# Kernel optimization log

Hardware: AMD Instinct MI355X
Metric: run time of the kernel (lower is better)

The kernel has to match this reference:

```python
import jax, jax.numpy as jnp
import numpy as np


def setup_inputs() -> dict:
    key = jax.random.key(0)
    k1, k2, k3, k4, k5 = jax.random.split(key, 5)
    B, S, H, L = 32, 4096, 512, 2
    scale = 1.0 / np.sqrt(H)
    return {
        "out": jax.random.normal(k1, (B, S, H), dtype=jnp.float32),
        "hidden": jax.random.normal(k2, (L, B, H), dtype=jnp.float32),
        "W": jax.random.normal(k3, (H, H), dtype=jnp.float32) * scale,
        "b": jax.random.normal(k4, (H,), dtype=jnp.float32) * scale,
        "v": jax.random.normal(k5, (H,), dtype=jnp.float32) * scale,
    }


def reference(out, hidden, W, b, v):
    # hidden_last: (B, 1, H) from last layer
    h_last = hidden[-1][:, None, :]
    # energy = tanh(out @ W^T + b + h_last)  -> (B, S, H)
    energy = jnp.tanh(jnp.einsum("bsh,oh->bso", out, W) + b + h_last)
    # scores = energy @ v  -> (B, S)
    scores = jnp.einsum("bsh,h->bs", energy, v)
    attn = jax.nn.softmax(scores, axis=-1)
    # context = sum_s attn[b,s] * out[b,s,:]  -> (B, H)
    context = jnp.einsum("bs,bsh->bh", attn, out)
    return (context, attn)
```

## Files before the change

### kernel.cpp

```cpp
#include <hip/hip_runtime.h>
#include <hip/hip_bf16.h>

#define B_ 32
#define S_ 4096
#define H_ 512
#define M_ (B_ * S_)
#define L_ 2

typedef __bf16 bf16;
typedef bf16 bf16x8 __attribute__((ext_vector_type(8)));
typedef float floatx4 __attribute__((ext_vector_type(4)));
typedef float floatx16 __attribute__((ext_vector_type(16)));

__device__ inline bf16 f2b(float f) { return (bf16)f; }

__device__ inline float fast_tanh(float x) {
    float xc = fminf(15.0f, fmaxf(-15.0f, x));
    float e = __expf(2.0f * xc);
    return (e - 1.0f) * __builtin_amdgcn_rcpf(e + 1.0f);
}

__global__ __launch_bounds__(256) void convert_Wfrag(const float* __restrict__ W,
                                                     bf16* __restrict__ Wf) {
    int gid  = blockIdx.x * 256 + threadIdx.x;
    int lane = gid & 63;
    int ks   = (gid >> 6) & 31;
    int nt   = gid >> 11;
    int row  = nt * 32 + (lane & 31);
    int col  = ks * 16 + (lane >> 5) * 8;
    const float* src = W + (size_t)row * H_ + col;
    floatx4 f0 = *(const floatx4*)src;
    floatx4 f1 = *(const floatx4*)(src + 4);
    bf16x8 p = { f2b(f0[0]), f2b(f0[1]), f2b(f0[2]), f2b(f0[3]),
                 f2b(f1[0]), f2b(f1[1]), f2b(f1[2]), f2b(f1[3]) };
    *(bf16x8*)(Wf + (size_t)gid * 8) = p;
}

#define MT 64

__global__ __launch_bounds__(256, 2) void scores_kernel(
    const float* __restrict__ outT,
    const bf16*  __restrict__ Wf,
    const float* __restrict__ bias,
    const float* __restrict__ hidden,
    const float* __restrict__ v,
    float* __restrict__ scores)
{
    __shared__ bf16 Alds[MT * 512];

    const int tid  = threadIdx.x;
    const int wave = tid >> 6;
    const int lane = tid & 63;
    const int l31  = lane & 31;
    const int half = lane >> 5;

    const int m0    = blockIdx.x * MT;
    const int batch = m0 >> 12;

    {
        const floatx4* src = (const floatx4*)(outT + (size_t)m0 * H_);
        #pragma unroll 4
        for (int it = 0; it < 16; ++it) {
            int idx = it * 256 + tid;
            int r   = idx >> 6;
            int j   = idx & 63;
            floatx4 f0 = __builtin_nontemporal_load(src + idx * 2);
            floatx4 f1 = __builtin_nontemporal_load(src + idx * 2 + 1);
            bf16x8 p = { f2b(f0[0]), f2b(f0[1]), f2b(f0[2]), f2b(f0[3]),
                         f2b(f1[0]), f2b(f1[1]), f2b(f1[2]), f2b(f1[3]) };
            int frag = (r >> 5) * 32 + (j >> 1);
            int slot = (j & 1) * 32 + ((r + (j >> 1)) & 31);
            *(bf16x8*)&Alds[frag * 512 + slot * 8] = p;
        }
    }
    __syncthreads();

    const bf16* wf = Wf + (size_t)(wave * 4) * 32 * 512 + lane * 8;

    floatx16 acc[2][4];
    #pragma unroll
    for (int mt = 0; mt < 2; ++mt)
        #pragma unroll
        for (int nt = 0; nt < 4; ++nt)
            acc[mt][nt] = (floatx16)(0.0f);

    bf16x8 bb[4][4];
    bf16x8 aa[2][2];
    #pragma unroll
    for (int p = 0; p < 4; ++p)
        #pragma unroll
        for (int nt = 0; nt < 4; ++nt)
            bb[p][nt] = *(const bf16x8*)(wf + nt * 16384 + p * 512);
    #pragma unroll
    for (int mt = 0; mt < 2; ++mt)
        aa[0][mt] = *(const bf16x8*)
            &Alds[(mt * 32 + 0) * 512 + (half * 32 + (l31 & 31)) * 8];

    #pragma unroll
    for (int ks = 0; ks < 32; ++ks) {
        const int cur = ks & 3;
        const int ap  = ks & 1;
        if (ks < 31) {
            const int rot = (l31 + ks + 1) & 31;
            #pragma unroll
            for (int mt = 0; mt < 2; ++mt)
                aa[ap ^ 1][mt] = *(const bf16x8*)
                    &Alds[(mt * 32 + ks + 1) * 512 + (half * 32 + rot) * 8];
        }
        #pragma unroll
        for (int mt = 0; mt < 2; ++mt)
            #pragma unroll
            for (int nt = 0; nt < 4; ++nt)
                acc[mt][nt] = __builtin_amdgcn_mfma_f32_32x32x16_bf16(
                    aa[ap][mt], bb[cur][nt], acc[mt][nt], 0, 0, 0);
        if (ks < 28) {
            #pragma unroll
            for (int nt = 0; nt < 4; ++nt)
                bb[cur][nt] = *(const bf16x8*)(wf + nt * 16384 + (ks + 4) * 512);
        }
    }

    const float* hlast = hidden + (size_t)((L_ - 1) * B_ + batch) * H_;
    float part[2][16];
    #pragma unroll
    for (int mt = 0; mt < 2; ++mt)
        #pragma unroll
        for (int rg = 0; rg < 16; ++rg) part[mt][rg] = 0.0f;

    #pragma unroll
    for (int nt = 0; nt < 4; ++nt) {
        int n = wave * 128 + nt * 32 + l31;
        float bn = bias[n] + hlast[n];
        float vn = v[n];
        #pragma unroll
        for (int mt = 0; mt < 2; ++mt)
            #pragma unroll
            for (int rg = 0; rg < 16; ++rg)
                part[mt][rg] += fast_tanh(acc[mt][nt][rg] + bn) * vn;
    }

    __syncthreads();
    float* sred = (float*)Alds;
    #pragma unroll
    for (int mt = 0; mt < 2; ++mt)
        #pragma unroll
        for (int rg = 0; rg < 16; ++rg) {
            float s = part[mt][rg];
            s += __shfl_xor(s, 1);
            s += __shfl_xor(s, 2);
            s += __shfl_xor(s, 4);
            s += __shfl_xor(s, 8);
            s += __shfl_xor(s, 16);
            if (l31 == 0) {
                int row = (rg & 3) + 8 * (rg >> 2) + 4 * half;
                sred[wave * 64 + mt * 32 + row] = s;
            }
        }
    __syncthreads();
    if (tid < 64)
        scores[m0 + tid] = (sred[tid] + sred[64 + tid]) + (sred[128 + tid] + sred[192 + tid]);
}

__global__ __launch_bounds__(256) void softmax_kernel(const float* __restrict__ scores,
                                                      float* __restrict__ attn) {
    __shared__ float red[4];
    int b = blockIdx.x, tid = threadIdx.x;
    const float* row = scores + (size_t)b * S_;
    float vals[16];
    float mx = -3.4e38f;
    #pragma unroll
    for (int i = 0; i < 16; ++i) { vals[i] = row[i * 256 + tid]; mx = fmaxf(mx, vals[i]); }
    #pragma unroll
    for (int off = 32; off >= 1; off >>= 1) mx = fmaxf(mx, __shfl_xor(mx, off));
    if ((tid & 63) == 0) red[tid >> 6] = mx;
    __syncthreads();
    mx = fmaxf(fmaxf(red[0], red[1]), fmaxf(red[2], red[3]));
    __syncthreads();
    float sum = 0.f;
    #pragma unroll
    for (int i = 0; i < 16; ++i) { vals[i] = __expf(vals[i] - mx); sum += vals[i]; }
    #pragma unroll
    for (int off = 32; off >= 1; off >>= 1) sum += __shfl_xor(sum, off);
    if ((tid & 63) == 0) red[tid >> 6] = sum;
    __syncthreads();
    float inv = 1.0f / (red[0] + red[1] + red[2] + red[3]);
    #pragma unroll
    for (int i = 0; i < 16; ++i) attn[(size_t)b * S_ + i * 256 + tid] = vals[i] * inv;
}

#define CS 256
__global__ __launch_bounds__(256) void context_partial(const float* __restrict__ outT,
                                                       const float* __restrict__ attn,
                                                       float* __restrict__ partial) {
    __shared__ float red[2][512];
    int b  = blockIdx.y;
    int sb = blockIdx.x;
    int tid = threadIdx.x;
    int h4 = tid & 127;
    int sg = tid >> 7;

    const floatx4* bp = (const floatx4*)(outT + ((size_t)b * S_ + sb * CS + sg * 128) * H_) + h4;
    const float*   ar = attn + (size_t)b * S_ + sb * CS + sg * 128;

    floatx4 a0 = (floatx4)(0.0f), a1 = a0, a2 = a0, a3 = a0;
    #pragma unroll 2
    for (int j = 0; j < 128; j += 4) {
        float w0 = ar[j + 0], w1 = ar[j + 1], w2 = ar[j + 2], w3 = ar[j + 3];
        a0 += w0 * __builtin_nontemporal_load(bp + (size_t)(j + 0) * 128);
        a1 += w1 * __builtin_nontemporal_load(bp + (size_t)(j + 1) * 128);
        a2 += w2 * __builtin_nontemporal_load(bp + (size_t)(j + 2) * 128);
        a3 += w3 * __builtin_nontemporal_load(bp + (size_t)(j + 3) * 128);
    }
    floatx4 a = (a0 + a1) + (a2 + a3);
    *(floatx4*)&red[sg][h4 * 4] = a;
    __syncthreads();
    if (tid < 128) {
        floatx4 r = *(floatx4*)&red[0][tid * 4] + *(floatx4*)&red[1][tid * 4];
        *(floatx4*)&partial[((size_t)b * 16 + sb) * H_ + tid * 4] = r;
    }
}

__global__ __launch_bounds__(256) void context_final(const float* __restrict__ partial,
                                                     float* __restrict__ ctx) {
    int gid = blockIdx.x * 256 + threadIdx.x;
    int b = gid >> 9, h = gid & 511;
    float s = 0.f;
    #pragma unroll
    for (int k = 0; k < 16; ++k) s += partial[((size_t)b * 16 + k) * H_ + h];
    ctx[gid] = s;
}

extern "C" void kernel_launch(void* const* d_in, const int* in_sizes, int n_in,
                              void* d_out, int out_size, void* d_ws, size_t ws_size,
                              hipStream_t stream) {
    const float* outT   = (const float*)d_in[0];
    const float* hidden = (const float*)d_in[1];
    const float* W      = (const float*)d_in[2];
    const float* bias   = (const float*)d_in[3];
    const float* v      = (const float*)d_in[4];

    float* ctx    = (float*)d_out;
    float* attn   = (float*)d_out + B_ * H_;
    float* scores  = (float*)d_ws;
    bf16*  Wf      = (bf16*)((char*)d_ws + (size_t)M_ * 4);
    float* partial = (float*)((char*)d_ws + (size_t)M_ * 4 + H_ * H_ * 2);

    convert_Wfrag<<<128, 256, 0, stream>>>(W, Wf);
    scores_kernel<<<M_ / MT, 256, 0, stream>>>(outT, Wf, bias, hidden, v, scores);
    softmax_kernel<<<B_, 256, 0, stream>>>(scores, attn);
    context_partial<<<dim3(S_ / CS, B_), 256, 0, stream>>>(outT, attn, partial);
    context_final<<<B_ * H_ / 256, 256, 0, stream>>>(partial, ctx);
}
```

Baseline: 458.9 us.

## Fuse context accumulation into scores kernel using per-tile online softmax partials

The scores kernel now computes a tile-local max and exp-sum for its 64 rows. Right after the scores are ready, it accumulates a partial context vector by re-reading its own just-loaded tile of `out`, which should still be cache-resident. This removes the separate context_partial pass, which streamed the whole `out` tensor from memory a second time. A new context_final rescales the 64 per-tile partials of each batch by exp(localmax - globalmax) and normalises by the combined sum. The cost is extra per-block work and a serialized tail in the scores kernel, plus a larger workspace for per-tile partials.

```diff
diff --git a/kernel.cpp b/kernel.cpp
--- a/kernel.cpp
+++ b/kernel.cpp
@@ -44,7 +44,10 @@
     const float* __restrict__ bias,
     const float* __restrict__ hidden,
     const float* __restrict__ v,
-    float* __restrict__ scores)
+    float* __restrict__ scores,
+    float* __restrict__ pc,
+    float* __restrict__ lmaxg,
+    float* __restrict__ lsumg)
 {
     __shared__ bf16 Alds[MT * 512];
 
@@ -141,6 +144,7 @@
 
     __syncthreads();
     float* sred = (float*)Alds;
+    float* pbuf = sred + 256;
     #pragma unroll
     for (int mt = 0; mt < 2; ++mt)
         #pragma unroll
@@ -157,8 +161,34 @@
             }
         }
     __syncthreads();
-    if (tid < 64)
-        scores[m0 + tid] = (sred[tid] + sred[64 + tid]) + (sred[128 + tid] + sred[192 + tid]);
+
+    if (tid < 64) {
+        float sc = (sred[tid] + sred[64 + tid]) + (sred[128 + tid] + sred[192 + tid]);
+        scores[m0 + tid] = sc;
+        float mx = sc;
+        #pragma unroll
+        for (int off = 32; off >= 1; off >>= 1) mx = fmaxf(mx, __shfl_xor(mx, off));
+        float p = __expf(sc - mx);
+        pbuf[tid] = p;
+        float sm = p;
+        #pragma unroll
+        for (int off = 32; off >= 1; off >>= 1) sm += __shfl_xor(sm, off);
+        if (tid == 0) { lmaxg[blockIdx.x] = mx; lsumg[blockIdx.x] = sm; }
+    }
+    __syncthreads();
+
+    {
+        const float2* op = (const float2*)(outT + (size_t)m0 * H_) + tid;
+        float2 a = {0.0f, 0.0f};
+        #pragma unroll 8
+        for (int s = 0; s < 64; ++s) {
+            float2 o = op[s * 256];
+            float ps = pbuf[s];
+            a.x += ps * o.x;
+            a.y += ps * o.y;
+        }
+        *(float2*)&pc[(size_t)blockIdx.x * H_ + tid * 2] = a;
+    }
 }
 
 __global__ __launch_bounds__(256) void softmax_kernel(const float* __restrict__ scores,
@@ -188,46 +218,38 @@
     for (int i = 0; i < 16; ++i) attn[(size_t)b * S_ + i * 256 + tid] = vals[i] * inv;
 }
 
-#define CS 256
-__global__ __launch_bounds__(256) void context_partial(const float* __restrict__ outT,
-                                                       const float* __restrict__ attn,
-                                                       float* __restrict__ partial) {
-    __shared__ float red[2][512];
-    int b  = blockIdx.y;
-    int sb = blockIdx.x;
-    int tid = threadIdx.x;
-    int h4 = tid & 127;
-    int sg = tid >> 7;
-
-    const floatx4* bp = (const floatx4*)(outT + ((size_t)b * S_ + sb * CS + sg * 128) * H_) + h4;
-    const float*   ar = attn + (size_t)b * S_ + sb * CS + sg * 128;
-
-    floatx4 a0 = (floatx4)(0.0f), a1 = a0, a2 = a0, a3 = a0;
-    #pragma unroll 2
-    for (int j = 0; j < 128; j += 4) {
-        float w0 = ar[j + 0], w1 = ar[j + 1], w2 = ar[j + 2], w3 = ar[j + 3];
-        a0 += w0 * __builtin_nontemporal_load(bp + (size_t)(j + 0) * 128);
-        a1 += w1 * __builtin_nontemporal_load(bp + (size_t)(j + 1) * 128);
-        a2 += w2 * __builtin_nontemporal_load(bp + (size_t)(j + 2) * 128);
-        a3 += w3 * __builtin_nontemporal_load(bp + (size_t)(j + 3) * 128);
-    }
-    floatx4 a = (a0 + a1) + (a2 + a3);
-    *(floatx4*)&red[sg][h4 * 4] = a;
-    __syncthreads();
-    if (tid < 128) {
-        floatx4 r = *(floatx4*)&red[0][tid * 4] + *(floatx4*)&red[1][tid * 4];
-        *(floatx4*)&partial[((size_t)b * 16 + sb) * H_ + tid * 4] = r;
-    }
-}
-
-__global__ __launch_bounds__(256) void context_final(const float* __restrict__ partial,
+__global__ __launch_bounds__(256) void context_final(const float* __restrict__ pc,
+                                                     const float* __restrict__ lmaxg,
+                                                     const float* __restrict__ lsumg,
                                                      float* __restrict__ ctx) {
-    int gid = blockIdx.x * 256 + threadIdx.x;
-    int b = gid >> 9, h = gid & 511;
-    float s = 0.f;
-    #pragma unroll
-    for (int k = 0; k < 16; ++k) s += partial[((size_t)b * 16 + k) * H_ + h];
-    ctx[gid] = s;
+    __shared__ float e_sh[64];
+    __shared__ float inv_sh;
+    int b = blockIdx.x, tid = threadIdx.x;
+    if (tid < 64) {
+        float lm = lmaxg[b * 64 + tid];
+        float mx = lm;
+        #pragma unroll
+        for (int off = 32; off >= 1; off >>= 1) mx = fmaxf(mx, __shfl_xor(mx, off));
+        float e = __expf(lm - mx);
+        e_sh[tid] = e;
+        float gs = e * lsumg[b * 64 + tid];
+        #pragma unroll
+        for (int off = 32; off >= 1; off >>= 1) gs += __shfl_xor(gs, off);
+        if (tid == 0) inv_sh = 1.0f / gs;
+    }
+    __syncthreads();
+    float inv = inv_sh;
+    const float2* pp = (const float2*)(pc + (size_t)b * 64 * H_) + tid;
+    float2 a = {0.0f, 0.0f};
+    #pragma unroll 8
+    for (int j = 0; j < 64; ++j) {
+        float2 q = pp[j * 256];
+        float e = e_sh[j];
+        a.x += e * q.x;
+        a.y += e * q.y;
+    }
+    float2 r = { a.x * inv, a.y * inv };
+    *(float2*)&ctx[(size_t)b * H_ + tid * 2] = r;
 }
 
 extern "C" void kernel_launch(void* const* d_in, const int* in_sizes, int n_in,
@@ -241,13 +263,17 @@
 
     float* ctx    = (float*)d_out;
     float* attn   = (float*)d_out + B_ * H_;
-    float* scores  = (float*)d_ws;
-    bf16*  Wf      = (bf16*)((char*)d_ws + (size_t)M_ * 4);
-    float* partial = (float*)((char*)d_ws + (size_t)M_ * 4 + H_ * H_ * 2);
+
+    const int NBLK = M_ / MT;
+    float* scores = (float*)d_ws;
+    bf16*  Wf     = (bf16*)((char*)d_ws + (size_t)M_ * 4);
+    float* pc     = (float*)((char*)d_ws + (size_t)M_ * 4 + (size_t)H_ * H_ * 2);
+    float* lmaxg  = pc + (size_t)NBLK * H_;
+    float* lsumg  = lmaxg + NBLK;
 
     convert_Wfrag<<<128, 256, 0, stream>>>(W, Wf);
-    scores_kernel<<<M_ / MT, 256, 0, stream>>>(outT, Wf, bias, hidden, v, scores);
+    scores_kernel<<<NBLK, 256, 0, stream>>>(outT, Wf, bias, hidden, v,
+                                            scores, pc, lmaxg, lsumg);
     softmax_kernel<<<B_, 256, 0, stream>>>(scores, attn);
-    context_partial<<<dim3(S_ / CS, B_), 256, 0, stream>>>(outT, attn, partial);
-    context_final<<<B_ * H_ / 256, 256, 0, stream>>>(partial, ctx);
-}
+    context_final<<<B_, 256, 0, stream>>>(pc, lmaxg, lsumg, ctx);
+}
```

Result: slower. 485.4 us (+5.8%).
